# Kernel tuning notes

Measured on AMD Instinct MI355X. Metric: run time of the kernel, lower is better.

Reference implementation:

```python
import jax, jax.numpy as jnp
import numpy as np

NEG_INF = jnp.float32(-1e9)  # finite large-negative avoids -inf*0 NaNs in grads


def setup_inputs() -> dict:
    key = jax.random.key(0)
    k1, k2, k3, k4, k5 = jax.random.split(key, 5)
    B, T, S, D = 16, 1024, 2048, 1024
    source = jax.random.normal(k1, (B, T, D), dtype=jnp.float32)
    memory_bank = jax.random.normal(k2, (B, S, D), dtype=jnp.float32)
    memory_lengths = jax.random.randint(k3, (B,), 1, S + 1, dtype=jnp.int32)
    # torch nn.Linear weights are [out_features, in_features]
    W_in = jax.random.normal(k4, (D, D), dtype=jnp.float32) / jnp.sqrt(jnp.float32(D))
    W_out = jax.random.normal(k5, (D, 2 * D), dtype=jnp.float32) / jnp.sqrt(jnp.float32(2 * D))
    return {"source": source, "memory_bank": memory_bank,
            "memory_lengths": memory_lengths, "W_in": W_in, "W_out": W_out}


def reference(source, memory_bank, memory_lengths, W_in, W_out):
    # GlobalAttention(attn_type='general', attn_func='softmax'), multi-step path
    B, T, D = source.shape
    S = memory_bank.shape[1]
    # score: general -> linear_in(h_t) @ h_s^T
    h_t = jnp.einsum('btd,ed->bte', source, W_in)            # [B,T,D]
    align = jnp.einsum('bte,bse->bts', h_t, memory_bank)      # [B,T,S]
    # sequence_mask on memory_lengths, broadcast over target dim
    mask = jnp.arange(S, dtype=jnp.int32)[None, None, :] < memory_lengths[:, None, None]
    align = jnp.where(mask, align, NEG_INF)
    align_vectors = jax.nn.softmax(align, axis=-1)            # [B,T,S]
    c = jnp.einsum('bts,bsd->btd', align_vectors, memory_bank)  # [B,T,D]
    concat_c = jnp.concatenate([c, source], axis=-1)          # [B,T,2D]
    attn_h = jnp.einsum('btf,of->bto', concat_c, W_out)       # linear_out, no bias for 'general'
    attn_h = jnp.tanh(attn_h)
    # not one_step -> transpose to [T,B,*]
    return attn_h.transpose(1, 0, 2), align_vectors.transpose(1, 0, 2)
```

## Files before the change

### kernel.cpp

```cpp
#include <hip/hip_runtime.h>

typedef __attribute__((ext_vector_type(8))) short s16x8;
typedef __attribute__((ext_vector_type(4))) float f32x4;
typedef __attribute__((ext_vector_type(4))) unsigned short u16x4;
typedef unsigned short u16;

__device__ __forceinline__ u16 f2bf(float x) {
  unsigned u = __builtin_bit_cast(unsigned, x);
  u = u + 0x7fffu + ((u >> 16) & 1u);
  return (u16)(u >> 16);
}
__device__ __forceinline__ float bf2f(u16 h) {
  return __builtin_bit_cast(float, (unsigned)h << 16);
}
__device__ __forceinline__ void split_bf(float x, u16 &h, u16 &l) {
  h = f2bf(x); l = f2bf(x - bf2f(h));
}

typedef __attribute__((address_space(1))) const unsigned int as1c_u32;
typedef __attribute__((address_space(3))) unsigned int as3_u32;
__device__ __forceinline__ void gload16(const void* g, void* l) {
  __builtin_amdgcn_global_load_lds((as1c_u32*)g, (as3_u32*)l, 16, 0, 0);
}

__global__ __launch_bounds__(256) void split_copy_k(
    const float* __restrict__ in, u16* __restrict__ oh, u16* __restrict__ ol, long n4) {
  const long i = (long)blockIdx.x * 256 + threadIdx.x;
  if (i >= n4) return;
  const f32x4 v = *(const f32x4*)(in + i * 4);
  u16x4 h, l;
#pragma unroll
  for (int e = 0; e < 4; ++e) { u16 hh, ll; split_bf(v[e], hh, ll); h[e] = hh; l[e] = ll; }
  *(u16x4*)(oh + i * 4) = h;
  *(u16x4*)(ol + i * 4) = l;
}

__global__ __launch_bounds__(256) void split_hi_k(
    const float* __restrict__ in, u16* __restrict__ oh, long n4) {
  const long i = (long)blockIdx.x * 256 + threadIdx.x;
  if (i >= n4) return;
  const f32x4 v = *(const f32x4*)(in + i * 4);
  u16x4 h;
#pragma unroll
  for (int e = 0; e < 4; ++e) h[e] = f2bf(v[e]);
  *(u16x4*)(oh + i * 4) = h;
}

__global__ __launch_bounds__(256) void transpose_bf_k(
    const u16* __restrict__ in, u16* __restrict__ outT) {
  __shared__ u16 tile[64][72];
  const int b = blockIdx.z;
  const int s0 = blockIdx.x * 64, d0 = blockIdx.y * 64;
  const u16* pin = in + (long)b * 2048 * 1024;
  u16* pout = outT + (long)b * 1024 * 2048;
  const int t = threadIdx.x;
#pragma unroll
  for (int i = 0; i < 4; ++i) {
    const int idx = i * 256 + t;
    const int r = idx >> 4;
    const int c4 = (idx & 15) * 4;
    *(u16x4*)&tile[r][c4] = *(const u16x4*)&pin[(long)(s0 + r) * 1024 + d0 + c4];
  }
  __syncthreads();
#pragma unroll
  for (int i = 0; i < 4; ++i) {
    const int idx = i * 256 + t;
    const int r = idx >> 4;
    const int c4 = (idx & 15) * 4;
    u16x4 v = { tile[c4][r], tile[c4 + 1][r], tile[c4 + 2][r], tile[c4 + 3][r] };
    *(u16x4*)&pout[(long)(d0 + r) * 2048 + s0 + c4] = v;
  }
}

__global__ __launch_bounds__(256) void softmax_k(
    float* __restrict__ alignBuf, const int* __restrict__ lens, float* __restrict__ outP) {
  const int row = blockIdx.x;
  const int b = row >> 10;
  const int tt = row & 1023;
  const int len = lens[b];
  float* arow = alignBuf + (long)row * 2048;
  const int t = threadIdx.x;
  const int lane = t & 63, wv = t >> 6;
  float v[8];
  float mx = -3.0e38f;
#pragma unroll
  for (int j = 0; j < 8; ++j) {
    const int s = j * 256 + t;
    float x = arow[s];
    x = (s < len) ? x : -1.0e9f;
    v[j] = x;
    mx = fmaxf(mx, x);
  }
#pragma unroll
  for (int off = 32; off; off >>= 1) mx = fmaxf(mx, __shfl_xor(mx, off));
  __shared__ float redm[4], reds[4];
  if (lane == 0) redm[wv] = mx;
  __syncthreads();
  mx = fmaxf(fmaxf(redm[0], redm[1]), fmaxf(redm[2], redm[3]));
  float e[8]; float sum = 0.f;
#pragma unroll
  for (int j = 0; j < 8; ++j) { e[j] = __expf(v[j] - mx); sum += e[j]; }
#pragma unroll
  for (int off = 32; off; off >>= 1) sum += __shfl_xor(sum, off);
  if (lane == 0) reds[wv] = sum;
  __syncthreads();
  sum = reds[0] + reds[1] + reds[2] + reds[3];
  const float inv = 1.0f / sum;
  u16* ph = (u16*)arow;
  u16* pl = ph + 2048;
  float* orow = outP + ((long)tt * 16 + b) * 2048;
#pragma unroll
  for (int j = 0; j < 8; ++j) {
    const int s = j * 256 + t;
    const float pv = e[j] * inv;
    orow[s] = pv;
    u16 h, l; split_bf(pv, h, l);
    ph[s] = h; pl[s] = l;
  }
}

template<int NPROD, int EP, int MASK>
__global__ __launch_bounds__(256) void gemm128(
    const u16* __restrict__ Ah, const u16* __restrict__ Al,
    const u16* __restrict__ Ah2, const u16* __restrict__ Al2,
    int kSplitA, int lda, long sA,
    const u16* __restrict__ Bh, const u16* __restrict__ Bl, int ldb, long sB,
    int K, const int* __restrict__ lens,
    float* __restrict__ Cf, u16* __restrict__ Ch, u16* __restrict__ Cl,
    int ldc, long sC, int lgx, int lgxy, int nwg) {
  constexpr int NT = (NPROD >= 3) ? 4 : (NPROD == 2 ? 3 : 2);
  __shared__ __align__(16) u16 lds[NT][4096];

  const int orig = blockIdx.x;
  const int wg = (orig & 7) * (nwg >> 3) + (orig >> 3);
  const int bx = wg & ((1 << lgx) - 1);
  const int by = (wg >> lgx) & ((1 << (lgxy - lgx)) - 1);
  const int bz = wg >> lgxy;

  const long m0 = (long)by * 128;
  const long n0 = (long)bx * 128;

  int Klim = K;
  if constexpr (MASK == 1) {
    if (n0 >= lens[bz]) return;
  } else if constexpr (MASK == 2) {
    const int kl = (lens[bz] + 31) & ~31;
    Klim = kl < K ? kl : K;
  }

  const u16* pAh  = Ah  + (long)bz * sA;
  const u16* pAl  = Al  + (long)bz * sA;
  const u16* pAh2 = Ah2 + (long)bz * sA;
  const u16* pAl2 = Al2 + (long)bz * sA;
  const u16* pBh  = Bh  + (long)bz * sB;
  const u16* pBl  = Bl  + (long)bz * sB;

  const int t = threadIdx.x;
  const int lane = t & 63;
  const int wv = t >> 6;
  const int wm = wv >> 1;
  const int wn = wv & 1;
  const int lk = lane >> 4;
  const int lr = lane & 15;

  f32x4 acc[4][4];
#pragma unroll
  for (int i = 0; i < 4; ++i)
#pragma unroll
    for (int j = 0; j < 4; ++j) acc[i][j] = 0.0f;

  for (int k0 = 0; k0 < Klim; k0 += 32) {
    __syncthreads();
#pragma unroll
    for (int j = 0; j < 2; ++j) {
      const int ci = (j * 4 + wv) * 64;
      const int c = ci + lane;
      const int kc = c >> 7;
      const int r = c & 127;
      const int k = k0 + kc * 8;
      const u16 *aH = pAh, *aL = pAl;
      long ka = k;
      if (k >= kSplitA) { aH = pAh2; aL = pAl2; ka = k - kSplitA; }
      const long aoff = (m0 + r) * (long)lda + ka;
      gload16(aH + aoff, &lds[0][ci * 8]);
      if constexpr (NPROD >= 2) gload16(aL + aoff, &lds[2][ci * 8]);
      const long boff = (n0 + r) * (long)ldb + k;
      gload16(pBh + boff, &lds[1][ci * 8]);
      if constexpr (NPROD >= 3) gload16(pBl + boff, &lds[3][ci * 8]);
    }
    __syncthreads();

    s16x8 ah[4], al[4], bh[4], bl[4];
#pragma unroll
    for (int f = 0; f < 4; ++f) {
      const int ra = wm * 64 + f * 16 + lr;
      const int rb = wn * 64 + f * 16 + lr;
      ah[f] = *(const s16x8*)&lds[0][lk * 1024 + ra * 8];
      bh[f] = *(const s16x8*)&lds[1][lk * 1024 + rb * 8];
      if constexpr (NPROD >= 2) al[f] = *(const s16x8*)&lds[2][lk * 1024 + ra * 8];
      if constexpr (NPROD >= 3) bl[f] = *(const s16x8*)&lds[3][lk * 1024 + rb * 8];
    }
#pragma unroll
    for (int i = 0; i < 4; ++i)
#pragma unroll
      for (int j = 0; j < 4; ++j) {
        acc[i][j] = __builtin_amdgcn_mfma_f32_16x16x32_bf16(ah[i], bh[j], acc[i][j], 0, 0, 0);
        if constexpr (NPROD >= 3)
          acc[i][j] = __builtin_amdgcn_mfma_f32_16x16x32_bf16(ah[i], bl[j], acc[i][j], 0, 0, 0);
        if constexpr (NPROD >= 2)
          acc[i][j] = __builtin_amdgcn_mfma_f32_16x16x32_bf16(al[i], bh[j], acc[i][j], 0, 0, 0);
      }
  }

#pragma unroll
  for (int fm = 0; fm < 4; ++fm)
#pragma unroll
    for (int fn = 0; fn < 4; ++fn)
#pragma unroll
      for (int r = 0; r < 4; ++r) {
        const long row = m0 + wm * 64 + fm * 16 + (lane >> 4) * 4 + r;
        const long col = n0 + wn * 64 + fn * 16 + lr;
        const float v = acc[fm][fn][r];
        if constexpr (EP == 0) {
          Cf[(long)bz * sC + row * ldc + col] = v;
        } else if constexpr (EP == 1) {
          u16 h, l; split_bf(v, h, l);
          const long o = (long)bz * sC + row * ldc + col;
          Ch[o] = h; Cl[o] = l;
        } else {
          const long bb = row >> 10;
          const long tt = row & 1023;
          Cf[(tt * 16 + bb) * (long)ldc + col] = tanhf(v);
        }
      }
}

extern "C" void kernel_launch(void* const* d_in, const int* in_sizes, int n_in,
                              void* d_out, int out_size, void* d_ws, size_t ws_size,
                              hipStream_t stream) {
  (void)in_sizes; (void)n_in; (void)out_size; (void)ws_size;
  const float* src = (const float*)d_in[0];
  const float* mb  = (const float*)d_in[1];
  const int*   lens= (const int*)d_in[2];
  const float* Wi  = (const float*)d_in[3];
  const float* Wo  = (const float*)d_in[4];
  float* out = (float*)d_out;

  char* p = (char*)d_ws;
  u16* mbS_hi  = (u16*)p;
  u16* mbS_lo  = (u16*)(p + (64L << 20));
  u16* srcU_hi = (u16*)(p + (128L << 20));
  u16* srcU_lo = (u16*)(p + (160L << 20));
  u16* htc_hi  = (u16*)(p + (192L << 20));
  u16* htc_lo  = (u16*)(p + (224L << 20));
  float* alignBuf = (float*)(p + (256L << 20));
  u16* Wi_hi = (u16*)alignBuf;
  u16* Wi_lo = Wi_hi + 1048576;
  u16* mbT   = mbS_lo;
  u16* Wo_hi = mbS_hi;

  dim3 blk(256);
  split_copy_k<<<dim3(32768), blk, 0, stream>>>(mb,  mbS_hi, mbS_lo, 8388608L);
  split_copy_k<<<dim3(16384), blk, 0, stream>>>(src, srcU_hi, srcU_lo, 4194304L);
  split_copy_k<<<dim3(1024),  blk, 0, stream>>>(Wi,  Wi_hi,  Wi_lo,  262144L);

  gemm128<3, 1, 0><<<dim3(1024), blk, 0, stream>>>(
      srcU_hi, srcU_lo, srcU_hi, srcU_lo, 1 << 30, 1024, 0L,
      Wi_hi, Wi_lo, 1024, 0L,
      1024, lens,
      nullptr, htc_hi, htc_lo, 1024, 0L,
      3, 10, 1024);

  gemm128<3, 0, 1><<<dim3(2048), blk, 0, stream>>>(
      htc_hi, htc_lo, htc_hi, htc_lo, 1 << 30, 1024, 1048576L,
      mbS_hi, mbS_lo, 1024, 2097152L,
      1024, lens,
      alignBuf, nullptr, nullptr, 2048, 2097152L,
      4, 7, 2048);

  softmax_k<<<dim3(16384), blk, 0, stream>>>(alignBuf, lens, out + 16777216L);

  transpose_bf_k<<<dim3(32, 16, 16), blk, 0, stream>>>(mbS_hi, mbT);
  split_hi_k<<<dim3(2048), blk, 0, stream>>>(Wo, Wo_hi, 524288L);

  gemm128<2, 1, 2><<<dim3(1024), blk, 0, stream>>>(
      (const u16*)alignBuf, (const u16*)alignBuf + 2048,
      (const u16*)alignBuf, (const u16*)alignBuf + 2048, 1 << 30, 4096, 4194304L,
      mbT, mbT, 2048, 2097152L,
      2048, lens,
      nullptr, htc_hi, htc_lo, 1024, 1048576L,
      3, 6, 1024);

  gemm128<2, 2, 0><<<dim3(1024), blk, 0, stream>>>(
      htc_hi, htc_lo, srcU_hi, srcU_lo, 1024, 1024, 0L,
      Wo_hi, Wo_hi, 2048, 0L,
      2048, lens,
      out, nullptr, nullptr, 1024, 0L,
      3, 10, 1024);
}
```

Measured before the change: 969.4 us.

## Use BK=64 tiles and single-bf16 operands for context and output GEMMs

Adds a BK template parameter so each k-iteration loads a 64-deep tile, halving the number of barrier-separated steps for the last two GEMMs. The context GEMM now writes only a bf16 hi value through a new epilogue instead of a hi/lo split. The output projection drops the lo-term product and runs as a single bf16 MFMA (NPROD=1). This cuts MFMA count and memory traffic, at the cost of lower precision in the context vector and attn_h and more LDS per block.

After: 886.9 us. 8.5% less time.

```diff
diff --git a/kernel.cpp b/kernel.cpp
--- a/kernel.cpp
+++ b/kernel.cpp
@@ -119,7 +119,7 @@
   }
 }
 
-template<int NPROD, int EP, int MASK>
+template<int NPROD, int EP, int MASK, int BK>
 __global__ __launch_bounds__(256) void gemm128(
     const u16* __restrict__ Ah, const u16* __restrict__ Al,
     const u16* __restrict__ Ah2, const u16* __restrict__ Al2,
@@ -129,7 +129,7 @@
     float* __restrict__ Cf, u16* __restrict__ Ch, u16* __restrict__ Cl,
     int ldc, long sC, int lgx, int lgxy, int nwg) {
   constexpr int NT = (NPROD >= 3) ? 4 : (NPROD == 2 ? 3 : 2);
-  __shared__ __align__(16) u16 lds[NT][4096];
+  __shared__ __align__(16) u16 lds[NT][128 * BK];
 
   const int orig = blockIdx.x;
   const int wg = (orig & 7) * (nwg >> 3) + (orig >> 3);
@@ -144,7 +144,7 @@
   if constexpr (MASK == 1) {
     if (n0 >= lens[bz]) return;
   } else if constexpr (MASK == 2) {
-    const int kl = (lens[bz] + 31) & ~31;
+    const int kl = (lens[bz] + BK - 1) & ~(BK - 1);
     Klim = kl < K ? kl : K;
   }
 
@@ -169,10 +169,10 @@
 #pragma unroll
     for (int j = 0; j < 4; ++j) acc[i][j] = 0.0f;
 
-  for (int k0 = 0; k0 < Klim; k0 += 32) {
+  for (int k0 = 0; k0 < Klim; k0 += BK) {
     __syncthreads();
 #pragma unroll
-    for (int j = 0; j < 2; ++j) {
+    for (int j = 0; j < BK / 16; ++j) {
       const int ci = (j * 4 + wv) * 64;
       const int c = ci + lane;
       const int kc = c >> 7;
@@ -190,26 +190,30 @@
     }
     __syncthreads();
 
-    s16x8 ah[4], al[4], bh[4], bl[4];
-#pragma unroll
-    for (int f = 0; f < 4; ++f) {
-      const int ra = wm * 64 + f * 16 + lr;
-      const int rb = wn * 64 + f * 16 + lr;
-      ah[f] = *(const s16x8*)&lds[0][lk * 1024 + ra * 8];
-      bh[f] = *(const s16x8*)&lds[1][lk * 1024 + rb * 8];
-      if constexpr (NPROD >= 2) al[f] = *(const s16x8*)&lds[2][lk * 1024 + ra * 8];
-      if constexpr (NPROD >= 3) bl[f] = *(const s16x8*)&lds[3][lk * 1024 + rb * 8];
+#pragma unroll
+    for (int ks = 0; ks < BK / 32; ++ks) {
+      const int fb = (ks * 4 + lk) * 1024;
+      s16x8 ah[4], al[4], bh[4], bl[4];
+#pragma unroll
+      for (int f = 0; f < 4; ++f) {
+        const int ra = wm * 64 + f * 16 + lr;
+        const int rb = wn * 64 + f * 16 + lr;
+        ah[f] = *(const s16x8*)&lds[0][fb + ra * 8];
+        bh[f] = *(const s16x8*)&lds[1][fb + rb * 8];
+        if constexpr (NPROD >= 2) al[f] = *(const s16x8*)&lds[2][fb + ra * 8];
+        if constexpr (NPROD >= 3) bl[f] = *(const s16x8*)&lds[3][fb + rb * 8];
+      }
+#pragma unroll
+      for (int i = 0; i < 4; ++i)
+#pragma unroll
+        for (int j = 0; j < 4; ++j) {
+          acc[i][j] = __builtin_amdgcn_mfma_f32_16x16x32_bf16(ah[i], bh[j], acc[i][j], 0, 0, 0);
+          if constexpr (NPROD >= 3)
+            acc[i][j] = __builtin_amdgcn_mfma_f32_16x16x32_bf16(ah[i], bl[j], acc[i][j], 0, 0, 0);
+          if constexpr (NPROD >= 2)
+            acc[i][j] = __builtin_amdgcn_mfma_f32_16x16x32_bf16(al[i], bh[j], acc[i][j], 0, 0, 0);
+        }
     }
-#pragma unroll
-    for (int i = 0; i < 4; ++i)
-#pragma unroll
-      for (int j = 0; j < 4; ++j) {
-        acc[i][j] = __builtin_amdgcn_mfma_f32_16x16x32_bf16(ah[i], bh[j], acc[i][j], 0, 0, 0);
-        if constexpr (NPROD >= 3)
-          acc[i][j] = __builtin_amdgcn_mfma_f32_16x16x32_bf16(ah[i], bl[j], acc[i][j], 0, 0, 0);
-        if constexpr (NPROD >= 2)
-          acc[i][j] = __builtin_amdgcn_mfma_f32_16x16x32_bf16(al[i], bh[j], acc[i][j], 0, 0, 0);
-      }
   }
 
 #pragma unroll
@@ -227,10 +231,12 @@
           u16 h, l; split_bf(v, h, l);
           const long o = (long)bz * sC + row * ldc + col;
           Ch[o] = h; Cl[o] = l;
-        } else {
+        } else if constexpr (EP == 2) {
           const long bb = row >> 10;
           const long tt = row & 1023;
           Cf[(tt * 16 + bb) * (long)ldc + col] = tanhf(v);
+        } else {
+          Ch[(long)bz * sC + row * ldc + col] = f2bf(v);
         }
       }
 }
@@ -264,14 +270,14 @@
   split_copy_k<<<dim3(16384), blk, 0, stream>>>(src, srcU_hi, srcU_lo, 4194304L);
   split_copy_k<<<dim3(1024),  blk, 0, stream>>>(Wi,  Wi_hi,  Wi_lo,  262144L);
 
-  gemm128<3, 1, 0><<<dim3(1024), blk, 0, stream>>>(
+  gemm128<3, 1, 0, 32><<<dim3(1024), blk, 0, stream>>>(
       srcU_hi, srcU_lo, srcU_hi, srcU_lo, 1 << 30, 1024, 0L,
       Wi_hi, Wi_lo, 1024, 0L,
       1024, lens,
       nullptr, htc_hi, htc_lo, 1024, 0L,
       3, 10, 1024);
 
-  gemm128<3, 0, 1><<<dim3(2048), blk, 0, stream>>>(
+  gemm128<3, 0, 1, 32><<<dim3(2048), blk, 0, stream>>>(
       htc_hi, htc_lo, htc_hi, htc_lo, 1 << 30, 1024, 1048576L,
       mbS_hi, mbS_lo, 1024, 2097152L,
       1024, lens,
@@ -283,16 +289,16 @@
   transpose_bf_k<<<dim3(32, 16, 16), blk, 0, stream>>>(mbS_hi, mbT);
   split_hi_k<<<dim3(2048), blk, 0, stream>>>(Wo, Wo_hi, 524288L);
 
-  gemm128<2, 1, 2><<<dim3(1024), blk, 0, stream>>>(
+  gemm128<2, 3, 2, 64><<<dim3(1024), blk, 0, stream>>>(
       (const u16*)alignBuf, (const u16*)alignBuf + 2048,
       (const u16*)alignBuf, (const u16*)alignBuf + 2048, 1 << 30, 4096, 4194304L,
       mbT, mbT, 2048, 2097152L,
       2048, lens,
-      nullptr, htc_hi, htc_lo, 1024, 1048576L,
+      nullptr, htc_hi, htc_hi, 1024, 1048576L,
       3, 6, 1024);
 
-  gemm128<2, 2, 0><<<dim3(1024), blk, 0, stream>>>(
-      htc_hi, htc_lo, srcU_hi, srcU_lo, 1024, 1024, 0L,
+  gemm128<1, 2, 0, 64><<<dim3(1024), blk, 0, stream>>>(
+      htc_hi, htc_hi, srcU_hi, srcU_hi, 1024, 1024, 0L,
       Wo_hi, Wo_hi, 2048, 0L,
       2048, lens,
       out, nullptr, nullptr, 1024, 0L,
```

## Add K=64 GEMM variant and drop lo-split precision in final two GEMMs

Applied to the files above, without the earlier changes.

Adds a gemm128w kernel that stages K=64 per iteration with double-size LDS tiles, halving the loop and barrier count. The context GEMM now writes only a bf16 hi output (no lo term), and the output projection uses a single bf16 product instead of hi/lo compensation. This cuts MFMA work, memory traffic and synchronisation, but lowers accuracy of the context vector and output projection and raises LDS use per block.

Result: faster. 883.6 us (-8.9%).

```diff
diff --git a/kernel.cpp b/kernel.cpp
--- a/kernel.cpp
+++ b/kernel.cpp
@@ -143,9 +143,6 @@
   int Klim = K;
   if constexpr (MASK == 1) {
     if (n0 >= lens[bz]) return;
-  } else if constexpr (MASK == 2) {
-    const int kl = (lens[bz] + 31) & ~31;
-    Klim = kl < K ? kl : K;
   }
 
   const u16* pAh  = Ah  + (long)bz * sA;
@@ -227,10 +224,120 @@
           u16 h, l; split_bf(v, h, l);
           const long o = (long)bz * sC + row * ldc + col;
           Ch[o] = h; Cl[o] = l;
-        } else {
+        }
+      }
+}
+
+template<int NPROD, int EP, int MASK>
+__global__ __launch_bounds__(256) void gemm128w(
+    const u16* __restrict__ Ah, const u16* __restrict__ Al,
+    const u16* __restrict__ Ah2, const u16* __restrict__ Al2,
+    int kSplitA, int lda, long sA,
+    const u16* __restrict__ Bh, const u16* __restrict__ Bl, int ldb, long sB,
+    int K, const int* __restrict__ lens,
+    float* __restrict__ Cf, u16* __restrict__ Ch, u16* __restrict__ Cl,
+    int ldc, long sC, int lgx, int lgxy, int nwg) {
+  constexpr int NT = (NPROD >= 3) ? 4 : (NPROD == 2 ? 3 : 2);
+  __shared__ __align__(16) u16 lds[NT][8192];
+
+  const int orig = blockIdx.x;
+  const int wg = (orig & 7) * (nwg >> 3) + (orig >> 3);
+  const int bx = wg & ((1 << lgx) - 1);
+  const int by = (wg >> lgx) & ((1 << (lgxy - lgx)) - 1);
+  const int bz = wg >> lgxy;
+
+  const long m0 = (long)by * 128;
+  const long n0 = (long)bx * 128;
+
+  int Klim = K;
+  if constexpr (MASK == 2) {
+    const int kl = (lens[bz] + 63) & ~63;
+    Klim = kl < K ? kl : K;
+  }
+
+  const u16* pAh  = Ah  + (long)bz * sA;
+  const u16* pAl  = Al  + (long)bz * sA;
+  const u16* pAh2 = Ah2 + (long)bz * sA;
+  const u16* pAl2 = Al2 + (long)bz * sA;
+  const u16* pBh  = Bh  + (long)bz * sB;
+  const u16* pBl  = Bl  + (long)bz * sB;
+
+  const int t = threadIdx.x;
+  const int lane = t & 63;
+  const int wv = t >> 6;
+  const int wm = wv >> 1;
+  const int wn = wv & 1;
+  const int lk = lane >> 4;
+  const int lr = lane & 15;
+
+  f32x4 acc[4][4];
+#pragma unroll
+  for (int i = 0; i < 4; ++i)
+#pragma unroll
+    for (int j = 0; j < 4; ++j) acc[i][j] = 0.0f;
+
+  for (int k0 = 0; k0 < Klim; k0 += 64) {
+    __syncthreads();
+#pragma unroll
+    for (int j = 0; j < 4; ++j) {
+      const int ci = (j * 4 + wv) * 64;
+      const int c = ci + lane;
+      const int kc = c >> 7;
+      const int r = c & 127;
+      const int k = k0 + kc * 8;
+      const u16 *aH = pAh, *aL = pAl;
+      long ka = k;
+      if (k >= kSplitA) { aH = pAh2; aL = pAl2; ka = k - kSplitA; }
+      const long aoff = (m0 + r) * (long)lda + ka;
+      gload16(aH + aoff, &lds[0][ci * 8]);
+      if constexpr (NPROD >= 2) gload16(aL + aoff, &lds[2][ci * 8]);
+      const long boff = (n0 + r) * (long)ldb + k;
+      gload16(pBh + boff, &lds[1][ci * 8]);
+      if constexpr (NPROD >= 3) gload16(pBl + boff, &lds[3][ci * 8]);
+    }
+    __syncthreads();
+
+#pragma unroll
+    for (int ks = 0; ks < 2; ++ks) {
+      const int fb = (ks * 4 + lk) * 1024;
+      s16x8 ah[4], al[4], bh[4], bl[4];
+#pragma unroll
+      for (int f = 0; f < 4; ++f) {
+        const int ra = wm * 64 + f * 16 + lr;
+        const int rb = wn * 64 + f * 16 + lr;
+        ah[f] = *(const s16x8*)&lds[0][fb + ra * 8];
+        bh[f] = *(const s16x8*)&lds[1][fb + rb * 8];
+        if constexpr (NPROD >= 2) al[f] = *(const s16x8*)&lds[2][fb + ra * 8];
+        if constexpr (NPROD >= 3) bl[f] = *(const s16x8*)&lds[3][fb + rb * 8];
+      }
+#pragma unroll
+      for (int i = 0; i < 4; ++i)
+#pragma unroll
+        for (int j = 0; j < 4; ++j) {
+          acc[i][j] = __builtin_amdgcn_mfma_f32_16x16x32_bf16(ah[i], bh[j], acc[i][j], 0, 0, 0);
+          if constexpr (NPROD >= 3)
+            acc[i][j] = __builtin_amdgcn_mfma_f32_16x16x32_bf16(ah[i], bl[j], acc[i][j], 0, 0, 0);
+          if constexpr (NPROD >= 2)
+            acc[i][j] = __builtin_amdgcn_mfma_f32_16x16x32_bf16(al[i], bh[j], acc[i][j], 0, 0, 0);
+        }
+    }
+  }
+
+#pragma unroll
+  for (int fm = 0; fm < 4; ++fm)
+#pragma unroll
+    for (int fn = 0; fn < 4; ++fn)
+#pragma unroll
+      for (int r = 0; r < 4; ++r) {
+        const long row = m0 + wm * 64 + fm * 16 + (lane >> 4) * 4 + r;
+        const long col = n0 + wn * 64 + fn * 16 + lr;
+        const float v = acc[fm][fn][r];
+        if constexpr (EP == 2) {
           const long bb = row >> 10;
           const long tt = row & 1023;
           Cf[(tt * 16 + bb) * (long)ldc + col] = tanhf(v);
+        } else {
+          Ch[(long)bz * sC + row * ldc + col] = f2bf(v);
         }
       }
 }
@@ -283,16 +390,16 @@
   transpose_bf_k<<<dim3(32, 16, 16), blk, 0, stream>>>(mbS_hi, mbT);
   split_hi_k<<<dim3(2048), blk, 0, stream>>>(Wo, Wo_hi, 524288L);
 
-  gemm128<2, 1, 2><<<dim3(1024), blk, 0, stream>>>(
+  gemm128w<2, 3, 2><<<dim3(1024), blk, 0, stream>>>(
       (const u16*)alignBuf, (const u16*)alignBuf + 2048,
       (const u16*)alignBuf, (const u16*)alignBuf + 2048, 1 << 30, 4096, 4194304L,
       mbT, mbT, 2048, 2097152L,
       2048, lens,
-      nullptr, htc_hi, htc_lo, 1024, 1048576L,
+      nullptr, htc_hi, htc_hi, 1024, 1048576L,
       3, 6, 1024);
 
-  gemm128<2, 2, 0><<<dim3(1024), blk, 0, stream>>>(
-      htc_hi, htc_lo, srcU_hi, srcU_lo, 1024, 1024, 0L,
+  gemm128w<1, 2, 0><<<dim3(1024), blk, 0, stream>>>(
+      htc_hi, htc_hi, srcU_hi, srcU_hi, 1024, 1024, 0L,
       Wo_hi, Wo_hi, 2048, 0L,
       2048, lens,
       out, nullptr, nullptr, 1024, 0L,
```
